# Kernel tuning notes

Measured on AMD Instinct MI355X. Metric: run time of the kernel, lower is better.

## Reference

```python
import jax, jax.numpy as jnp
import numpy as np

B, H, W = 2, 32, 128
HW = H * W
N, C = 4096, 64
KQ, KN = 32, 16          # nsample_q, nsample
DIST = 10.0              # neighbor distance threshold
NEG = -1e10


def _knn(q, p, k):
    # q: (B,M,3), p: (B,N,3) -> idx (B,M,k), sqdist (B,M,k)
    sqd = jnp.sum((q[:, :, None, :] - p[:, None, :, :]) ** 2, axis=-1)
    neg, idx = jax.lax.top_k(-sqd, k)
    return idx, -neg


def _gather(p, idx):
    # p: (B,N,C), idx: (B,M,K) -> (B,M,K,C)
    return jax.vmap(lambda a, i: a[i])(p, idx)


def _norm_feat(x):
    # per-point channel normalization, torch.std default is unbiased (ddof=1)
    m = jnp.mean(x, axis=-1, keepdims=True)
    s = jnp.clip(jnp.std(x, axis=-1, keepdims=True, ddof=1), 1e-12)
    return (x - m) / s


def _conv(x, w, b, g, e):
    # 1x1 conv + BatchNorm (track_running_stats=False -> batch stats) + LeakyReLU(0.1)
    y = jnp.einsum('bnkc,cd->bnkd', x, w) + b
    mu = y.mean(axis=(0, 1, 2), keepdims=True)
    var = y.var(axis=(0, 1, 2), keepdims=True)
    y = (y - mu) * jax.lax.rsqrt(var + 1e-5) * g + e
    return jnp.where(y > 0, y, 0.1 * y)


def setup_inputs() -> dict:
    key = jax.random.key(0)
    ks = jax.random.split(key, 20)
    inp = {
        'xyz_proj_raw': jax.random.normal(ks[0], (B, H, W, 3), jnp.float32),
        'warped_xyz': jax.random.normal(ks[1], (B, HW, 3), jnp.float32),
        'warped_points': jax.random.normal(ks[2], (B, HW, C), jnp.float32),
        'idx_n2': jax.random.randint(ks[3], (B, HW, 2), 0, W),
        'f2_xyz': jax.random.normal(ks[4], (B, N, 3), jnp.float32),
        'f2_points': jax.random.normal(ks[5], (B, N, C), jnp.float32),
        'lidar_z': jax.random.uniform(ks[6], (B, HW, 1), jnp.float32),
    }
    shapes = {
        'm1w0': (70, 128), 'm1w1': (128, 64), 'piw': (6, 64),
        'm2w0': (128, 64), 'm2w1': (64, 64), 'pcw': (10, 64),
        'm3w0': (192, 64), 'm3w1': (64, 64),
    }
    i = 7
    for name, shp in shapes.items():
        inp[name] = jax.random.normal(ks[i], shp, jnp.float32) * 0.05
        i += 1
        pre = name[:-2] if name[-2] == 'w' else name[:-1]
        suf = name[-1] if name[-2] == 'w' else ''
        cout = shp[1]
        inp[pre + 'b' + suf] = jnp.zeros((cout,), jnp.float32)
        inp[pre + 'g' + suf] = jnp.ones((cout,), jnp.float32)
        inp[pre + 'e' + suf] = jnp.zeros((cout,), jnp.float32)
    return inp


def reference(xyz_proj_raw, warped_xyz, warped_points, idx_n2, f2_xyz, f2_points, lidar_z,
              m1w0, m1b0, m1g0, m1e0, m1w1, m1b1, m1g1, m1e1,
              piw, pib, pig, pie,
              m2w0, m2b0, m2g0, m2e0, m2w1, m2b1, m2g1, m2e1,
              pcw, pcb, pcg, pce,
              m3w0, m3b0, m3g0, m3e0, m3w1, m3b1, m3g1, m3e1):
    # ---- stage 1: cross kNN grouping into image features ----
    idx_q, _ = _knn(warped_xyz, f2_xyz, KQ)
    qi_xyz = _gather(f2_xyz, idx_q)          # (B,HW,KQ,3)
    qi_pts = _gather(f2_points, idx_q)       # (B,HW,KQ,C)

    wxyz = warped_xyz * lidar_z              # (B,HW,3)
    pi_xyz_exp = jnp.broadcast_to(wxyz[:, :, None, :], (B, HW, KQ, 3))
    pi_pts_exp = jnp.broadcast_to(warped_points[:, :, None, :], (B, HW, KQ, C))
    pi_xyz_diff_concat = jnp.concatenate([pi_xyz_exp, qi_xyz], axis=3)  # (B,HW,KQ,6)

    pi_feat_diff = _norm_feat(pi_pts_exp) * _norm_feat(qi_pts)          # correlation
    feat = jnp.concatenate([pi_xyz_diff_concat, pi_feat_diff], axis=3)  # (B,HW,KQ,70)

    feat = _conv(feat, m1w0, m1b0, m1g0, m1e0)
    feat = _conv(feat, m1w1, m1b1, m1g1, m1e1)                          # (B,HW,KQ,64)
    pi_enc = _conv(pi_xyz_diff_concat, piw, pib, pig, pie)              # (B,HW,KQ,64)

    pi_cat = jnp.concatenate([pi_enc, feat], axis=3)
    pi_cat = _conv(pi_cat, m2w0, m2b0, m2g0, m2e0)
    pi_cat = _conv(pi_cat, m2w1, m2b1, m2g1, m2e1)
    WQ = jax.nn.softmax(pi_cat, axis=2)
    pi_feat1 = jnp.sum(WQ * feat, axis=2)                               # (B,HW,64)

    # ---- stage 2: self kNN (use_trans=False -> raw projected xyz), thresholded validity ----
    xyz_pr = xyz_proj_raw.reshape(B, HW, 3)
    idx2, sqd2 = _knn(xyz_pr, xyz_pr, KN)
    valid = (sqd2 < DIST * DIST).astype(pi_feat1.dtype)[..., None]      # (B,HW,KN,1)

    pc_xyz_g = _gather(wxyz, idx2)                                      # (B,HW,KN,3)
    pc_pts_g = _gather(pi_feat1, idx2)                                  # (B,HW,KN,64)
    pc_xyz_new = jnp.broadcast_to(wxyz[:, :, None, :], (B, HW, KN, 3))
    pc_pts_new = jnp.broadcast_to(warped_points[:, :, None, :], (B, HW, KN, C))

    pc_diff = pc_xyz_g - pc_xyz_new
    pc_euc = jnp.sqrt(jnp.sum(pc_diff * pc_diff, axis=3, keepdims=True) + 1e-20)
    pc_xyz_cat = jnp.concatenate([pc_xyz_new, pc_xyz_g, pc_diff, pc_euc], axis=3)  # 10ch

    pc_enc = _conv(pc_xyz_cat, pcw, pcb, pcg, pce)
    pc_cat = jnp.concatenate([pc_enc, pc_pts_new, pc_pts_g], axis=-1)   # (B,HW,KN,192)
    pc_cat = _conv(pc_cat, m3w0, m3b0, m3g0, m3e0)
    pc_cat = _conv(pc_cat, m3w1, m3b1, m3g1, m3e1)

    pc_cat = pc_cat * valid + NEG * (1.0 - valid)
    WP = jax.nn.softmax(pc_cat, axis=2)
    out = jnp.sum(WP * pc_pts_g, axis=2)                                # (B,HW,64)
    return out.reshape(B, H, W, -1)
```

## Files before the change

### kernel.cpp

```cpp
#include <hip/hip_runtime.h>
#include <math.h>

constexpr int Bn  = 2;
constexpr int HWn = 4096;
constexpr int Nn  = 4096;
constexpr int KQn = 32;
constexpr int KNn = 16;
constexpr float INV_R1 = 1.0f/262144.0f;
constexpr float INV_R2 = 1.0f/131072.0f;

typedef _Float16 f16x8 __attribute__((ext_vector_type(8)));
typedef float    f32x4 __attribute__((ext_vector_type(4)));

__device__ __forceinline__ float wred64(float v){
  #pragma unroll
  for (int m = 32; m > 0; m >>= 1) v += __shfl_xor(v, m, 64);
  return v;
}
__device__ __forceinline__ float leakyf(float v){ return v > 0.f ? v : 0.1f*v; }

__device__ __forceinline__ void bn_param(const float* st, int c, float inv_n,
                                         const float* g, const float* e,
                                         float& sc, float& sh){
  float mu  = st[c]*inv_n;
  float var = st[128+c]*inv_n - mu*mu;
  float s   = g[c]*rsqrtf(var + 1e-5f);
  sc = s; sh = e[c] - mu*s;
}

__device__ __forceinline__ void build_x70(int row,
    const float* __restrict__ wxyz, const float* __restrict__ f2_xyz,
    const float* __restrict__ normW, const float* __restrict__ normF2,
    const int* __restrict__ idxq, float* x){
  int p = row >> 5;
  int b = p >> 12;
  int idx = idxq[row];
  const float* wx = wxyz + (size_t)p*3;
  const float* fx = f2_xyz + ((size_t)b*Nn + idx)*3;
  x[0]=wx[0]; x[1]=wx[1]; x[2]=wx[2];
  x[3]=fx[0]; x[4]=fx[1]; x[5]=fx[2];
  const float4* nw = (const float4*)(normW  + (size_t)p*64);
  const float4* nf = (const float4*)(normF2 + ((size_t)b*Nn + idx)*64);
  #pragma unroll
  for (int c=0;c<16;c++){
    float4 a = nw[c], q = nf[c];
    x[6+4*c+0]=a.x*q.x; x[6+4*c+1]=a.y*q.y; x[6+4*c+2]=a.z*q.z; x[6+4*c+3]=a.w*q.w;
  }
}

__device__ __forceinline__ void build_x10(int row,
    const float* __restrict__ wxyz, const int* __restrict__ idx2, float* x){
  int p = row >> 4, b = p >> 12;
  int idx = idx2[row];
  const float* nw = wxyz + (size_t)p*3;
  const float* gw = wxyz + ((size_t)b*HWn + idx)*3;
  float n0=nw[0],n1=nw[1],n2=nw[2];
  float g0=gw[0],g1=gw[1],g2=gw[2];
  float d0=g0-n0, d1=g1-n1, d2=g2-n2;
  x[0]=n0;x[1]=n1;x[2]=n2; x[3]=g0;x[4]=g1;x[5]=g2;
  x[6]=d0;x[7]=d1;x[8]=d2; x[9]=sqrtf(d0*d0+d1*d1+d2*d2+1e-20f);
}

__global__ __launch_bounds__(256) void k_prep(
    const float* __restrict__ warped_xyz, const float* __restrict__ lidar_z,
    const float* __restrict__ warped_points, const float* __restrict__ f2_points,
    const float* __restrict__ m1w0, const float* __restrict__ m1w1,
    const float* __restrict__ piw, const float* __restrict__ pcw,
    const float* __restrict__ m2w0, const float* __restrict__ m2w1,
    const float* __restrict__ m3w0, const float* __restrict__ m3w1,
    float* __restrict__ wxyz, float* __restrict__ normW, float* __restrict__ normF2,
    float* __restrict__ piwT, float* __restrict__ pcwT,
    _Float16* __restrict__ w1h, _Float16* __restrict__ w2h,
    _Float16* __restrict__ w3h, _Float16* __restrict__ w4h,
    _Float16* __restrict__ w5h, _Float16* __restrict__ w6h)
{
  int blk = blockIdx.x, tid = threadIdx.x;
  if (blk < 4096){
    int lane = tid & 63;
    int p = blk*4 + (tid >> 6);
    const float* src; float* dst;
    if (p < Bn*HWn){ src = warped_points + (size_t)p*64; dst = normW + (size_t)p*64; }
    else { int q = p - Bn*HWn; src = f2_points + (size_t)q*64; dst = normF2 + (size_t)q*64; }
    float x = src[lane];
    float m = wred64(x) * (1.f/64.f);
    float d = x - m;
    float ss = wred64(d*d);
    float s = fmaxf(sqrtf(ss*(1.f/63.f)), 1e-12f);
    dst[lane] = d / s;
  } else if (blk < 4192){
    int e = (blk-4096)*256 + tid;
    wxyz[e] = warped_xyz[e] * lidar_z[e/3];
  } else if (blk < 4196){
    int e = (blk-4192)*256 + tid;
    if (e < 384){ piwT[(e & 63)*6  + (e >> 6)] = piw[e]; }
    else if (e < 1024){ int f = e-384; pcwT[(f & 63)*10 + (f >> 6)] = pcw[f]; }
  } else {
    int e = (blk-4196)*256 + tid;
    if (e < 12288){
      int j = e/96, k = e - j*96;
      w1h[e] = (k < 70) ? (_Float16)m1w0[k*128 + j] : (_Float16)0.f;
    } else if (e < 20480){
      int f = e - 12288; int d = f >> 7, c = f & 127;
      w2h[f] = (_Float16)m1w1[c*64 + d];
    } else if (e < 28672){
      int f = e - 20480; int d = f >> 7, c = f & 127;
      w3h[f] = (_Float16)m2w0[c*64 + d];
    } else if (e < 32768){
      int f = e - 28672; int d = f >> 6, c = f & 63;
      w4h[f] = (_Float16)m2w1[c*64 + d];
    } else if (e < 45056){
      int f = e - 32768; int d = f/192, c = f - 192*d;
      w5h[f] = (_Float16)m3w0[c*64 + d];
    } else {
      int f = e - 45056; int d = f >> 6, c = f & 63;
      w6h[f] = (_Float16)m3w1[c*64 + d];
    }
  }
}

template<int K, bool WRITE_VALID>
__global__ __launch_bounds__(256) void k_knn(
    const float* __restrict__ qpts, const float* __restrict__ pts,
    int* __restrict__ oidx, float* __restrict__ ovalid)
{
  __shared__ int hist[4*256];
  __shared__ int wsum[4];
  __shared__ unsigned int redm[4], redM[4];
  __shared__ unsigned int sh_sel;
  __shared__ int sh_rem, sh_cls, cnt_lt, cnt_eq;
  int b = blockIdx.x >> 12;
  int qi = blockIdx.x & 4095;
  int tid = threadIdx.x;
  int lane = tid & 63, wv = tid >> 6;
  const float* qp = qpts + ((size_t)(b*HWn+qi))*3;
  float qx=qp[0], qy=qp[1], qz=qp[2];
  const float* pb = pts + (size_t)b*Nn*3;
  unsigned int key[16];
  #pragma unroll
  for (int i=0;i<16;i++){
    int t = tid + i*256;
    float dx = __fsub_rn(qx, pb[t*3+0]);
    float dy = __fsub_rn(qy, pb[t*3+1]);
    float dz = __fsub_rn(qz, pb[t*3+2]);
    float d2 = __fadd_rn(__fadd_rn(__fmul_rn(dx,dx), __fmul_rn(dy,dy)), __fmul_rn(dz,dz));
    key[i] = __float_as_uint(d2);
  }
  unsigned int mn = key[0], mx = key[0];
  #pragma unroll
  for (int i=1;i<16;i++){ mn = min(mn, key[i]); mx = max(mx, key[i]); }
  #pragma unroll
  for (int m=32;m>0;m>>=1){
    mn = min(mn, (unsigned int)__shfl_xor((int)mn, m, 64));
    mx = max(mx, (unsigned int)__shfl_xor((int)mx, m, 64));
  }
  if (lane == 0){ redm[wv] = mn; redM[wv] = mx; }
  if (tid == 0){ cnt_lt = 0; cnt_eq = 0; }
  __syncthreads();
  mn = min(min(redm[0],redm[1]), min(redm[2],redm[3]));
  mx = max(max(redM[0],redM[1]), max(redM[2],redM[3]));
  unsigned int R = mx - mn;
  int L = (R == 0u) ? 0 : (31 - __clz(R));
  int shift = (L > 7) ? (L - 7) : 0;
  unsigned int dmask = 255u;

  unsigned int active = 0xFFFFu, below = 0u;
  int rem = K;
  for (;;){
    __syncthreads();
    #pragma unroll
    for (int j=0;j<4;j++) hist[j*256 + tid] = 0;
    __syncthreads();
    #pragma unroll
    for (int i=0;i<16;i++){
      if (active & (1u<<i))
        atomicAdd(&hist[wv*256 + (int)(((key[i]-mn) >> shift) & dmask)], 1);
    }
    __syncthreads();
    int h = hist[tid] + hist[256+tid] + hist[512+tid] + hist[768+tid];
    int pref = h;
    #pragma unroll
    for (int m=1;m<64;m<<=1){ int t = __shfl_up(pref, m, 64); if (lane >= m) pref += t; }
    if (lane == 63) wsum[wv] = pref;
    __syncthreads();
    int off = 0;
    #pragma unroll
    for (int i=0;i<3;i++) if (i < wv) off += wsum[i];
    pref += off;
    if (pref >= rem && (pref - h) < rem){
      sh_sel = (unsigned int)tid;
      sh_rem = rem - (pref - h);
      sh_cls = h;
    }
    __syncthreads();
    unsigned int sel = sh_sel; rem = sh_rem; int cls = sh_cls;
    #pragma unroll
    for (int i=0;i<16;i++){
      if (active & (1u<<i)){
        unsigned int d = ((key[i]-mn) >> shift) & dmask;
        if (d < sel) below |= (1u<<i);
        if (d != sel) active &= ~(1u<<i);
      }
    }
    if (cls == rem || shift == 0) break;
    int w = (shift < 8) ? shift : 8;
    shift -= w;
    dmask = (w == 8) ? 255u : ((1u<<w) - 1u);
  }
  size_t obase = ((size_t)(b*HWn+qi))*K;
  int nless = K - rem;
  const unsigned int U100 = __float_as_uint(100.0f);
  #pragma unroll
  for (int i=0;i<16;i++){
    if (below & (1u<<i)){
      int s = atomicAdd(&cnt_lt, 1);
      oidx[obase+s] = tid + i*256;
      if constexpr (WRITE_VALID) ovalid[obase+s] = (key[i] < U100) ? 1.f : 0.f;
    } else if (active & (1u<<i)){
      int s = atomicAdd(&cnt_eq, 1);
      if (s < rem){
        oidx[obase+nless+s] = tid + i*256;
        if constexpr (WRITE_VALID) ovalid[obase+nless+s] = (key[i] < U100) ? 1.f : 0.f;
      }
    }
  }
}

__global__ __launch_bounds__(256) void k_buildX1(
    const float* __restrict__ wxyz, const float* __restrict__ f2_xyz,
    const float* __restrict__ normW, const float* __restrict__ normF2,
    const int* __restrict__ idxq, _Float16* __restrict__ X1)
{
  int row = blockIdx.x*256 + threadIdx.x;
  float x[70];
  build_x70(row, wxyz, f2_xyz, normW, normF2, idxq, x);
  unsigned int* d32 = (unsigned int*)(X1 + (size_t)row*96);
  union { unsigned int u; _Float16 h[2]; } pk;
  #pragma unroll
  for (int c=0;c<35;c++){
    pk.h[0] = (_Float16)x[2*c]; pk.h[1] = (_Float16)x[2*c+1];
    d32[c] = pk.u;
  }
  #pragma unroll
  for (int c=35;c<48;c++) d32[c] = 0u;
}

__global__ __launch_bounds__(256) void k_gram(
    const float* __restrict__ wxyz, const float* __restrict__ f2_xyz,
    const int* __restrict__ idxq, const int* __restrict__ idx2,
    float* __restrict__ gram)
{
  __shared__ float sacc[66];
  int blk = blockIdx.x, tid = threadIdx.x, lane = tid & 63;
  if (blk < 64){
    float a[28];
    #pragma unroll
    for (int q=0;q<28;q++) a[q]=0.f;
    int g = blk*256 + tid;
    for (int s=0;s<16;s++){
      int row = g + s*16384;
      int p = row >> 5, b = p >> 12;
      int idx = idxq[row];
      const float* wx = wxyz + (size_t)p*3;
      const float* fx = f2_xyz + ((size_t)b*Nn + idx)*3;
      float xt[7] = {wx[0],wx[1],wx[2],fx[0],fx[1],fx[2],1.f};
      int q=0;
      #pragma unroll
      for (int i=0;i<7;i++)
        #pragma unroll
        for (int j=i;j<7;j++) a[q++] += xt[i]*xt[j];
    }
    if (tid < 28) sacc[tid]=0.f;
    __syncthreads();
    #pragma unroll
    for (int q=0;q<28;q++){
      float v = wred64(a[q]);
      if (lane==0) atomicAdd(&sacc[q], v);
    }
    __syncthreads();
    if (tid < 28) atomicAdd(&gram[tid], sacc[tid]);
  } else {
    float a[66];
    #pragma unroll
    for (int q=0;q<66;q++) a[q]=0.f;
    int g = (blk-64)*256 + tid;
    for (int s=0;s<16;s++){
      int row = g + s*8192;
      float x[10];
      build_x10(row, wxyz, idx2, x);
      float xt[11] = {x[0],x[1],x[2],x[3],x[4],x[5],x[6],x[7],x[8],x[9],1.f};
      int q=0;
      #pragma unroll
      for (int i=0;i<11;i++)
        #pragma unroll
        for (int j=i;j<11;j++) a[q++] += xt[i]*xt[j];
    }
    if (tid < 66) sacc[tid]=0.f;
    __syncthreads();
    #pragma unroll
    for (int q=0;q<66;q++){
      float v = wred64(a[q]);
      if (lane==0) atomicAdd(&sacc[q], v);
    }
    __syncthreads();
    if (tid < 66) atomicAdd(&gram[32+tid], sacc[tid]);
  }
}

__global__ __launch_bounds__(128) void k_gram_fin(
    const float* __restrict__ gram,
    const float* __restrict__ piw, const float* __restrict__ pib,
    const float* __restrict__ pcw, const float* __restrict__ pcb,
    float* stats)
{
  int tid = threadIdx.x;
  if (tid < 64){
    int c = tid;
    float wt[7];
    #pragma unroll
    for (int i=0;i<6;i++) wt[i] = piw[i*64+c];
    wt[6] = pib[c];
    const float* G = gram;
    float sum=0.f, ssq=0.f;
    #pragma unroll
    for (int i=0;i<7;i++){
      int offi = i*7 - (i*(i-1))/2;
      sum += wt[i]*G[offi + (6-i)];
      #pragma unroll
      for (int j=0;j<7;j++){
        int ii = i<j? i : j, jj = i<j? j : i;
        int o = ii*7 - (ii*(ii-1))/2 + (jj-ii);
        ssq += wt[i]*wt[j]*G[o];
      }
    }
    stats[2*256+c] = sum; stats[2*256+128+c] = ssq;
  } else {
    int c = tid-64;
    float wt[11];
    #pragma unroll
    for (int i=0;i<10;i++) wt[i] = pcw[i*64+c];
    wt[10] = pcb[c];
    const float* G = gram + 32;
    float sum=0.f, ssq=0.f;
    #pragma unroll
    for (int i=0;i<11;i++){
      int offi = i*11 - (i*(i-1))/2;
      sum += wt[i]*G[offi + (10-i)];
      #pragma unroll
      for (int j=0;j<11;j++){
        int ii = i<j? i : j, jj = i<j? j : i;
        int o = ii*11 - (ii*(ii-1))/2 + (jj-ii);
        ssq += wt[i]*wt[j]*G[o];
      }
    }
    stats[5*256+c] = sum; stats[5*256+128+c] = ssq;
  }
}

__global__ __launch_bounds__(256) void k_mfma_stats1(
    const _Float16* __restrict__ X1, const _Float16* __restrict__ w1h,
    float* stats)
{
  __shared__ float ssum[128], sssq[128];
  int tid = threadIdx.x;
  if (tid < 128){ ssum[tid]=0.f; sssq[tid]=0.f; }
  __syncthreads();
  int wave = tid >> 6, lane = tid & 63;
  int quad = lane >> 4, n16 = lane & 15;
  float r1[8], r2[8];
  #pragma unroll
  for (int i=0;i<8;i++){ r1[i]=0.f; r2[i]=0.f; }
  for (int t=0;t<4;t++){
    int m0 = blockIdx.x*256 + t*64 + wave*16;
    const _Float16* xr = X1 + (size_t)(m0 + n16)*96 + quad*8;
    f16x8 a0 = *(const f16x8*)(xr);
    f16x8 a1 = *(const f16x8*)(xr + 32);
    f16x8 a2 = *(const f16x8*)(xr + 64);
    #pragma unroll
    for (int nt = 0; nt < 8; nt++){
      const _Float16* wr = w1h + (size_t)(nt*16 + n16)*96 + quad*8;
      f16x8 b0 = *(const f16x8*)(wr);
      f16x8 b1 = *(const f16x8*)(wr + 32);
      f16x8 b2 = *(const f16x8*)(wr + 64);
      f32x4 acc = {0.f,0.f,0.f,0.f};
      acc = __builtin_amdgcn_mfma_f32_16x16x32_f16(a0, b0, acc, 0,0,0);
      acc = __builtin_amdgcn_mfma_f32_16x16x32_f16(a1, b1, acc, 0,0,0);
      acc = __builtin_amdgcn_mfma_f32_16x16x32_f16(a2, b2, acc, 0,0,0);
      float s1 = acc[0]+acc[1]+acc[2]+acc[3];
      float s2 = acc[0]*acc[0]+acc[1]*acc[1]+acc[2]*acc[2]+acc[3]*acc[3];
      s1 += __shfl_xor(s1, 16, 64); s1 += __shfl_xor(s1, 32, 64);
      s2 += __shfl_xor(s2, 16, 64); s2 += __shfl_xor(s2, 32, 64);
      r1[nt] += s1; r2[nt] += s2;
    }
  }
  if (quad == 0){
    #pragma unroll
    for (int nt=0;nt<8;nt++){
      atomicAdd(&ssum[nt*16+n16], r1[nt]); atomicAdd(&sssq[nt*16+n16], r2[nt]);
    }
  }
  __syncthreads();
  if (tid < 128){ atomicAdd(&stats[tid], ssum[tid]); atomicAdd(&stats[128+tid], sssq[tid]); }
}

__global__ __launch_bounds__(256) void k_mfma_m1(
    const _Float16* __restrict__ X1, const _Float16* __restrict__ w1h,
    const _Float16* __restrict__ w2h,
    const float* __restrict__ m1g0, const float* __restrict__ m1e0,
    float* stats, _Float16* __restrict__ y2h)
{
  __shared__ _Float16 st[64*136];
  __shared__ float sc1[128], sh1[128], ssum[64], sssq[64];
  int tid = threadIdx.x;
  if (tid < 128){
    float s,h; bn_param(stats, tid, INV_R1, m1g0, m1e0, s, h);
    sc1[tid]=s; sh1[tid]=h;
  }
  if (tid < 64){ ssum[tid]=0.f; sssq[tid]=0.f; }
  __syncthreads();
  int wave = tid >> 6, lane = tid & 63;
  int quad = lane >> 4, n16 = lane & 15;
  float r1[4], r2[4];
  #pragma unroll
  for (int i=0;i<4;i++){ r1[i]=0.f; r2[i]=0.f; }
  for (int t=0;t<4;t++){
    int m0 = blockIdx.x*256 + t*64 + wave*16;
    const _Float16* xr = X1 + (size_t)(m0 + n16)*96 + quad*8;
    f16x8 a0 = *(const f16x8*)(xr);
    f16x8 a1 = *(const f16x8*)(xr + 32);
    f16x8 a2 = *(const f16x8*)(xr + 64);
    #pragma unroll
    for (int nt = 0; nt < 8; nt++){
      const _Float16* wr = w1h + (size_t)(nt*16 + n16)*96 + quad*8;
      f16x8 b0 = *(const f16x8*)(wr);
      f16x8 b1 = *(const f16x8*)(wr + 32);
      f16x8 b2 = *(const f16x8*)(wr + 64);
      f32x4 acc = {0.f,0.f,0.f,0.f};
      acc = __builtin_amdgcn_mfma_f32_16x16x32_f16(a0, b0, acc, 0,0,0);
      acc = __builtin_amdgcn_mfma_f32_16x16x32_f16(a1, b1, acc, 0,0,0);
      acc = __builtin_amdgcn_mfma_f32_16x16x32_f16(a2, b2, acc, 0,0,0);
      int ch = nt*16 + n16;
      float sc = sc1[ch], sh = sh1[ch];
      #pragma unroll
      for (int r=0;r<4;r++){
        float v = leakyf(acc[r]*sc + sh);
        st[(size_t)(wave*16 + quad*4 + r)*136 + ch] = (_Float16)v;
      }
    }
    __syncthreads();
    const _Float16* tr = st + (size_t)(wave*16 + n16)*136 + quad*8;
    f16x8 t0 = *(const f16x8*)(tr);
    f16x8 t1 = *(const f16x8*)(tr + 32);
    f16x8 t2 = *(const f16x8*)(tr + 64);
    f16x8 t3 = *(const f16x8*)(tr + 96);
    #pragma unroll
    for (int nt = 0; nt < 4; nt++){
      const _Float16* wr = w2h + (size_t)(nt*16 + n16)*128 + quad*8;
      f16x8 b0 = *(const f16x8*)(wr);
      f16x8 b1 = *(const f16x8*)(wr + 32);
      f16x8 b2 = *(const f16x8*)(wr + 64);
      f16x8 b3 = *(const f16x8*)(wr + 96);
      f32x4 acc = {0.f,0.f,0.f,0.f};
      acc = __builtin_amdgcn_mfma_f32_16x16x32_f16(t0, b0, acc, 0,0,0);
      acc = __builtin_amdgcn_mfma_f32_16x16x32_f16(t1, b1, acc, 0,0,0);
      acc = __builtin_amdgcn_mfma_f32_16x16x32_f16(t2, b2, acc, 0,0,0);
      acc = __builtin_amdgcn_mfma_f32_16x16x32_f16(t3, b3, acc, 0,0,0);
      int ch = nt*16 + n16;
      #pragma unroll
      for (int r=0;r<4;r++){
        int rowg = blockIdx.x*256 + t*64 + wave*16 + quad*4 + r;
        y2h[(size_t)rowg*64 + ch] = (_Float16)acc[r];
      }
      float s1 = acc[0]+acc[1]+acc[2]+acc[3];
      float s2 = acc[0]*acc[0]+acc[1]*acc[1]+acc[2]*acc[2]+acc[3]*acc[3];
      s1 += __shfl_xor(s1, 16, 64); s1 += __shfl_xor(s1, 32, 64);
      s2 += __shfl_xor(s2, 16, 64); s2 += __shfl_xor(s2, 32, 64);
      r1[nt] += s1; r2[nt] += s2;
    }
    __syncthreads();
  }
  if (quad == 0){
    #pragma unroll
    for (int nt=0;nt<4;nt++){
      atomicAdd(&ssum[nt*16+n16], r1[nt]); atomicAdd(&sssq[nt*16+n16], r2[nt]);
    }
  }
  __syncthreads();
  if (tid < 64){ atomicAdd(&stats[1*256+tid], ssum[tid]); atomicAdd(&stats[1*256+128+tid], sssq[tid]); }
}

__global__ __launch_bounds__(256) void k_mfma_m2a(
    const float* __restrict__ wxyz, const float* __restrict__ f2_xyz,
    const int* __restrict__ idxq,
    const float* __restrict__ piwT, const float* __restrict__ pib,
    const float* __restrict__ pig, const float* __restrict__ pie,
    const float* __restrict__ m1g1, const float* __restrict__ m1e1,
    const _Float16* __restrict__ y2h, const _Float16* __restrict__ w3h,
    float* stats, _Float16* __restrict__ y3h)
{
  __shared__ _Float16 su[64*136];
  __shared__ float spw[384];
  __shared__ float scp[64], shp[64], sc2[64], sh2[64], ssum[64], sssq[64];
  int tid = threadIdx.x;
  for (int d = tid; d < 384; d += 256) spw[d] = piwT[d];
  if (tid < 64){
    float s,h;
    bn_param(stats+2*256, tid, INV_R1, pig,  pie,  s, h); scp[tid]=s; shp[tid]=h;
    bn_param(stats+1*256, tid, INV_R1, m1g1, m1e1, s, h); sc2[tid]=s; sh2[tid]=h;
    ssum[tid]=0.f; sssq[tid]=0.f;
  }
  __syncthreads();
  int r = tid & 63, cg = tid >> 6;
  int wave = tid >> 6, lane = tid & 63, quad = lane >> 4, n16 = lane & 15;
  float r1[4], r2[4];
  #pragma unroll
  for (int i=0;i<4;i++){ r1[i]=0.f; r2[i]=0.f; }
  for (int t=0;t<4;t++){
    int rowg = blockIdx.x*256 + t*64 + r;
    {
      int p = rowg >> 5, b = p >> 12;
      int idx = idxq[rowg];
      const float* wx = wxyz + (size_t)p*3;
      const float* fx = f2_xyz + ((size_t)b*Nn + idx)*3;
      float x0=wx[0],x1=wx[1],x2=wx[2],x3=fx[0],x4=fx[1],x5=fx[2];
      #pragma unroll
      for (int jj=0;jj<16;jj++){
        int j = cg*16 + jj;
        const float* pw = spw + j*6;
        float e = pib[j] + x0*pw[0]+x1*pw[1]+x2*pw[2]+x3*pw[3]+x4*pw[4]+x5*pw[5];
        su[r*136 + j] = (_Float16)leakyf(e*scp[j] + shp[j]);
      }
      const f16x8* yr = (const f16x8*)(y2h + (size_t)rowg*64 + cg*16);
      f16x8 q0 = yr[0], q1 = yr[1];
      #pragma unroll
      for (int jj=0;jj<8;jj++){
        int c = cg*16 + jj;
        su[r*136 + 64 + c] = (_Float16)leakyf((float)q0[jj]*sc2[c] + sh2[c]);
      }
      #pragma unroll
      for (int jj=0;jj<8;jj++){
        int c = cg*16 + 8 + jj;
        su[r*136 + 64 + c] = (_Float16)leakyf((float)q1[jj]*sc2[c] + sh2[c]);
      }
    }
    __syncthreads();
    const _Float16* ur = su + (size_t)(wave*16 + n16)*136 + quad*8;
    f16x8 a0 = *(const f16x8*)(ur);
    f16x8 a1 = *(const f16x8*)(ur + 32);
    f16x8 a2 = *(const f16x8*)(ur + 64);
    f16x8 a3 = *(const f16x8*)(ur + 96);
    #pragma unroll
    for (int nt = 0; nt < 4; nt++){
      const _Float16* wr = w3h + (size_t)(nt*16 + n16)*128 + quad*8;
      f16x8 b0 = *(const f16x8*)(wr);
      f16x8 b1 = *(const f16x8*)(wr + 32);
      f16x8 b2 = *(const f16x8*)(wr + 64);
      f16x8 b3 = *(const f16x8*)(wr + 96);
      f32x4 acc = {0.f,0.f,0.f,0.f};
      acc = __builtin_amdgcn_mfma_f32_16x16x32_f16(a0, b0, acc, 0,0,0);
      acc = __builtin_amdgcn_mfma_f32_16x16x32_f16(a1, b1, acc, 0,0,0);
      acc = __builtin_amdgcn_mfma_f32_16x16x32_f16(a2, b2, acc, 0,0,0);
      acc = __builtin_amdgcn_mfma_f32_16x16x32_f16(a3, b3, acc, 0,0,0);
      int ch = nt*16 + n16;
      #pragma unroll
      for (int rr=0;rr<4;rr++){
        int rg = blockIdx.x*256 + t*64 + wave*16 + quad*4 + rr;
        y3h[(size_t)rg*64 + ch] = (_Float16)acc[rr];
      }
      float s1 = acc[0]+acc[1]+acc[2]+acc[3];
      float s2 = acc[0]*acc[0]+acc[1]*acc[1]+acc[2]*acc[2]+acc[3]*acc[3];
      s1 += __shfl_xor(s1, 16, 64); s1 += __shfl_xor(s1, 32, 64);
      s2 += __shfl_xor(s2, 16, 64); s2 += __shfl_xor(s2, 32, 64);
      r1[nt] += s1; r2[nt] += s2;
    }
    __syncthreads();
  }
  if (quad == 0){
    #pragma unroll
    for (int nt=0;nt<4;nt++){
      atomicAdd(&ssum[nt*16+n16], r1[nt]); atomicAdd(&sssq[nt*16+n16], r2[nt]);
    }
  }
  __syncthreads();
  if (tid < 64){ atomicAdd(&stats[3*256+tid], ssum[tid]); atomicAdd(&stats[3*256+128+tid], sssq[tid]); }
}

__global__ __launch_bounds__(256) void k_mfma_pw64(
    const _Float16* __restrict__ yin, const _Float16* __restrict__ wh,
    const float* __restrict__ g, const float* __restrict__ e,
    const float* statsIn, float* statsOut, float inv_n,
    _Float16* __restrict__ yout)
{
  __shared__ _Float16 stt[64*72];
  __shared__ float sc[64], sh[64], ssum[64], sssq[64];
  int tid = threadIdx.x;
  if (tid < 64){
    float s,h; bn_param(statsIn, tid, inv_n, g, e, s, h);
    sc[tid]=s; sh[tid]=h; ssum[tid]=0.f; sssq[tid]=0.f;
  }
  __syncthreads();
  int r = tid & 63, cg = tid >> 6;
  int wave = tid >> 6, lane = tid & 63, quad = lane >> 4, n16 = lane & 15;
  float r1[4], r2[4];
  #pragma unroll
  for (int i=0;i<4;i++){ r1[i]=0.f; r2[i]=0.f; }
  for (int t=0;t<4;t++){
    int rowg = blockIdx.x*256 + t*64 + r;
    const f16x8* yr = (const f16x8*)(yin + (size_t)rowg*64 + cg*16);
    f16x8 q0 = yr[0], q1 = yr[1];
    #pragma unroll
    for (int jj=0;jj<8;jj++){
      int c = cg*16 + jj;
      stt[r*72 + c] = (_Float16)leakyf((float)q0[jj]*sc[c] + sh[c]);
    }
    #pragma unroll
    for (int jj=0;jj<8;jj++){
      int c = cg*16 + 8 + jj;
      stt[r*72 + c] = (_Float16)leakyf((float)q1[jj]*sc[c] + sh[c]);
    }
    __syncthreads();
    const _Float16* tr = stt + (size_t)(wave*16 + n16)*72 + quad*8;
    f16x8 a0 = *(const f16x8*)(tr);
    f16x8 a1 = *(const f16x8*)(tr + 32);
    #pragma unroll
    for (int nt = 0; nt < 4; nt++){
      const _Float16* wr = wh + (size_t)(nt*16 + n16)*64 + quad*8;
      f16x8 b0 = *(const f16x8*)(wr);
      f16x8 b1 = *(const f16x8*)(wr + 32);
      f32x4 acc = {0.f,0.f,0.f,0.f};
      acc = __builtin_amdgcn_mfma_f32_16x16x32_f16(a0, b0, acc, 0,0,0);
      acc = __builtin_amdgcn_mfma_f32_16x16x32_f16(a1, b1, acc, 0,0,0);
      int ch = nt*16 + n16;
      #pragma unroll
      for (int rr=0;rr<4;rr++){
        int rg = blockIdx.x*256 + t*64 + wave*16 + quad*4 + rr;
        yout[(size_t)rg*64 + ch] = (_Float16)acc[rr];
      }
      float s1 = acc[0]+acc[1]+acc[2]+acc[3];
      float s2 = acc[0]*acc[0]+acc[1]*acc[1]+acc[2]*acc[2]+acc[3]*acc[3];
      s1 += __shfl_xor(s1, 16, 64); s1 += __shfl_xor(s1, 32, 64);
      s2 += __shfl_xor(s2, 16, 64); s2 += __shfl_xor(s2, 32, 64);
      r1[nt] += s1; r2[nt] += s2;
    }
    __syncthreads();
  }
  if (quad == 0){
    #pragma unroll
    for (int nt=0;nt<4;nt++){
      atomicAdd(&ssum[nt*16+n16], r1[nt]); atomicAdd(&sssq[nt*16+n16], r2[nt]);
    }
  }
  __syncthreads();
  if (tid < 64){ atomicAdd(&statsOut[tid], ssum[tid]); atomicAdd(&statsOut[128+tid], sssq[tid]); }
}

__global__ __launch_bounds__(256) void k_mfma_m3a(
    const float* __restrict__ wxyz, const float* __restrict__ warped_points,
    const _Float16* __restrict__ pif1h, const int* __restrict__ idx2,
    const float* __restrict__ pcwT, const float* __restrict__ pcb,
    const float* __restrict__ pcg, const float* __restrict__ pce,
    const _Float16* __restrict__ w5h,
    float* stats, _Float16* __restrict__ y5h)
{
  __shared__ _Float16 sv[64*200];
  __shared__ float spw[640];
  __shared__ float scp[64], shp[64], ssum[64], sssq[64];
  int tid = threadIdx.x;
  for (int d = tid; d < 640; d += 256) spw[d] = pcwT[d];
  if (tid < 64){
    float s,h; bn_param(stats+5*256, tid, INV_R2, pcg, pce, s, h);
    scp[tid]=s; shp[tid]=h; ssum[tid]=0.f; sssq[tid]=0.f;
  }
  __syncthreads();
  int r = tid & 63, cg = tid >> 6;
  int wave = tid >> 6, lane = tid & 63, quad = lane >> 4, n16 = lane & 15;
  float r1[4], r2[4];
  #pragma unroll
  for (int i=0;i<4;i++){ r1[i]=0.f; r2[i]=0.f; }
  for (int t=0;t<4;t++){
    int rowg = blockIdx.x*256 + t*64 + r;
    {
      int p = rowg >> 4, b = p >> 12;
      int idx = idx2[rowg];
      float x[10];
      build_x10(rowg, wxyz, idx2, x);
      #pragma unroll
      for (int jj=0;jj<16;jj++){
        int j = cg*16 + jj;
        const float* pw = spw + j*10;
        float e = pcb[j];
        #pragma unroll
        for (int i=0;i<10;i++) e += x[i]*pw[i];
        sv[r*200 + j] = (_Float16)leakyf(e*scp[j] + shp[j]);
      }
      const float4* wp = (const float4*)(warped_points + (size_t)p*64 + cg*16);
      #pragma unroll
      for (int v4=0; v4<4; v4++){
        float4 q = wp[v4];
        int c = 64 + cg*16 + v4*4;
        sv[r*200 + c + 0] = (_Float16)q.x;
        sv[r*200 + c + 1] = (_Float16)q.y;
        sv[r*200 + c + 2] = (_Float16)q.z;
        sv[r*200 + c + 3] = (_Float16)q.w;
      }
      const f16x8* pg = (const f16x8*)(pif1h + ((size_t)(b*HWn) + idx)*64 + cg*16);
      f16x8 g0 = pg[0], g1 = pg[1];
      #pragma unroll
      for (int jj=0;jj<8;jj++) sv[r*200 + 128 + cg*16 + jj] = g0[jj];
      #pragma unroll
      for (int jj=0;jj<8;jj++) sv[r*200 + 136 + cg*16 + jj] = g1[jj];
    }
    __syncthreads();
    const _Float16* vr = sv + (size_t)(wave*16 + n16)*200 + quad*8;
    f16x8 a0 = *(const f16x8*)(vr);
    f16x8 a1 = *(const f16x8*)(vr + 32);
    f16x8 a2 = *(const f16x8*)(vr + 64);
    f16x8 a3 = *(const f16x8*)(vr + 96);
    f16x8 a4 = *(const f16x8*)(vr + 128);
    f16x8 a5 = *(const f16x8*)(vr + 160);
    #pragma unroll
    for (int nt = 0; nt < 4; nt++){
      const _Float16* wr = w5h + (size_t)(nt*16 + n16)*192 + quad*8;
      f32x4 acc = {0.f,0.f,0.f,0.f};
      acc = __builtin_amdgcn_mfma_f32_16x16x32_f16(a0, *(const f16x8*)(wr),       acc, 0,0,0);
      acc = __builtin_amdgcn_mfma_f32_16x16x32_f16(a1, *(const f16x8*)(wr + 32),  acc, 0,0,0);
      acc = __builtin_amdgcn_mfma_f32_16x16x32_f16(a2, *(const f16x8*)(wr + 64),  acc, 0,0,0);
      acc = __builtin_amdgcn_mfma_f32_16x16x32_f16(a3, *(const f16x8*)(wr + 96),  acc, 0,0,0);
      acc = __builtin_amdgcn_mfma_f32_16x16x32_f16(a4, *(const f16x8*)(wr + 128), acc, 0,0,0);
      acc = __builtin_amdgcn_mfma_f32_16x16x32_f16(a5, *(const f16x8*)(wr + 160), acc, 0,0,0);
      int ch = nt*16 + n16;
      #pragma unroll
      for (int rr=0;rr<4;rr++){
        int rg = blockIdx.x*256 + t*64 + wave*16 + quad*4 + rr;
        y5h[(size_t)rg*64 + ch] = (_Float16)acc[rr];
      }
      float s1 = acc[0]+acc[1]+acc[2]+acc[3];
      float s2 = acc[0]*acc[0]+acc[1]*acc[1]+acc[2]*acc[2]+acc[3]*acc[3];
      s1 += __shfl_xor(s1, 16, 64); s1 += __shfl_xor(s1, 32, 64);
      s2 += __shfl_xor(s2, 16, 64); s2 += __shfl_xor(s2, 32, 64);
      r1[nt] += s1; r2[nt] += s2;
    }
    __syncthreads();
  }
  if (quad == 0){
    #pragma unroll
    for (int nt=0;nt<4;nt++){
      atomicAdd(&ssum[nt*16+n16], r1[nt]); atomicAdd(&sssq[nt*16+n16], r2[nt]);
    }
  }
  __syncthreads();
  if (tid < 64){ atomicAdd(&stats[6*256+tid], ssum[tid]); atomicAdd(&stats[6*256+128+tid], sssq[tid]); }
}

__global__ __launch_bounds__(256) void k_softmax1(
    const _Float16* __restrict__ y2h, const _Float16* __restrict__ y4h,
    const float* stats,
    const float* __restrict__ m1g1, const float* __restrict__ m1e1,
    const float* __restrict__ m2g1, const float* __restrict__ m2e1,
    _Float16* __restrict__ pif1h)
{
  int tid = threadIdx.x, lane = tid & 63;
  int p = blockIdx.x*4 + (tid >> 6);
  int d = lane;
  float sc2,sh2,sc4,sh4;
  bn_param(stats+1*256, d, INV_R1, m1g1, m1e1, sc2, sh2);
  bn_param(stats+4*256, d, INV_R1, m2g1, m2e1, sc4, sh4);
  size_t rb = (size_t)p*KQn;
  float v[32]; float mx = -1e30f;
  #pragma unroll
  for (int k=0;k<32;k++){
    float t = leakyf((float)y4h[(rb+k)*64 + d]*sc4 + sh4);
    v[k] = t; mx = fmaxf(mx, t);
  }
  float se = 0.f;
  #pragma unroll
  for (int k=0;k<32;k++){ float ev = __expf(v[k]-mx); v[k]=ev; se += ev; }
  float inv = 1.f/se, acc = 0.f;
  #pragma unroll
  for (int k=0;k<32;k++){
    float f = leakyf((float)y2h[(rb+k)*64 + d]*sc2 + sh2);
    acc += v[k]*f;
  }
  pif1h[(size_t)p*64 + d] = (_Float16)(acc*inv);
}

__global__ __launch_bounds__(256) void k_softmax2(
    const _Float16* __restrict__ y6h, const _Float16* __restrict__ pif1h,
    const int* __restrict__ idx2, const float* __restrict__ validf,
    const float* stats,
    const float* __restrict__ m3g1, const float* __restrict__ m3e1,
    float* __restrict__ out)
{
  int tid = threadIdx.x, lane = tid & 63;
  int p = blockIdx.x*4 + (tid >> 6);
  int b = p >> 12;
  int d = lane;
  float sc,sh; bn_param(stats+7*256, d, INV_R2, m3g1, m3e1, sc, sh);
  size_t rb = (size_t)p*KNn;
  float v[16]; float mx = -1e30f;
  #pragma unroll
  for (int k=0;k<16;k++){
    float t = leakyf((float)y6h[(rb+k)*64 + d]*sc + sh);
    t = (validf[rb+k] > 0.5f) ? t : -1e10f;
    v[k] = t; mx = fmaxf(mx, t);
  }
  float se = 0.f;
  #pragma unroll
  for (int k=0;k<16;k++){ float ev = __expf(v[k]-mx); v[k]=ev; se += ev; }
  float inv = 1.f/se, acc = 0.f;
  #pragma unroll
  for (int k=0;k<16;k++){
    int idx = idx2[rb+k];
    acc += v[k]*(float)pif1h[((size_t)(b*HWn) + idx)*64 + d];
  }
  out[(size_t)p*64 + d] = acc*inv;
}

extern "C" void kernel_launch(void* const* d_in, const int* in_sizes, int n_in,
                              void* d_out, int out_size, void* d_ws, size_t ws_size,
                              hipStream_t stream)
{
  (void)in_sizes; (void)n_in; (void)out_size; (void)ws_size;
  const float* xyz_proj      = (const float*)d_in[0];
  const float* warped_xyz    = (const float*)d_in[1];
  const float* warped_points = (const float*)d_in[2];
  const float* f2_xyz        = (const float*)d_in[4];
  const float* f2_points     = (const float*)d_in[5];
  const float* lidar_z       = (const float*)d_in[6];
  const float* m1w0=(const float*)d_in[7],  *m1g0=(const float*)d_in[9],  *m1e0=(const float*)d_in[10];
  const float* m1w1=(const float*)d_in[11], *m1g1=(const float*)d_in[13], *m1e1=(const float*)d_in[14];
  const float* piw =(const float*)d_in[15], *pib =(const float*)d_in[16], *pig =(const float*)d_in[17], *pie =(const float*)d_in[18];
  const float* m2w0=(const float*)d_in[19], *m2g0=(const float*)d_in[21], *m2e0=(const float*)d_in[22];
  const float* m2w1=(const float*)d_in[23], *m2g1=(const float*)d_in[25], *m2e1=(const float*)d_in[26];
  const float* pcw =(const float*)d_in[27], *pcb =(const float*)d_in[28], *pcg =(const float*)d_in[29], *pce =(const float*)d_in[30];
  const float* m3w0=(const float*)d_in[31], *m3g0=(const float*)d_in[33], *m3e0=(const float*)d_in[34];
  const float* m3w1=(const float*)d_in[35], *m3g1=(const float*)d_in[37], *m3e1=(const float*)d_in[38];
  float* out = (float*)d_out;

  float* ws     = (float*)d_ws;
  float* wxyz   = ws;
  float* normW  = wxyz   + 24576;
  float* normF2 = normW  + 524288;
  float* piwT   = normF2 + 524288;
  float* pcwT   = piwT   + 384;
  float* stats  = pcwT   + 640;
  float* gram   = stats  + 2048;
  int*   idxq   = (int*)(gram + 128);
  int*   idx2   = idxq   + 262144;
  float* validf = (float*)(idx2 + 131072);
  _Float16* pif1h = (_Float16*)(validf + 131072);
  float* X1f    = validf + 131072 + 524288;
  _Float16* X1  = (_Float16*)X1f;
  float* y2f    = X1f + 12582912;
  _Float16* y2h = (_Float16*)y2f;
  float* y3f    = y2f + 8388608;
  _Float16* y3h = (_Float16*)y3f;
  float* whb    = y3f + 8388608;
  _Float16* w1h = (_Float16*)whb;
  _Float16* w2h = w1h + 12288;
  _Float16* w3h = w2h + 8192;
  _Float16* w4h = w3h + 8192;
  _Float16* w5h = w4h + 4096;
  _Float16* w6h = w5h + 12288;
  _Float16* y4h = (_Float16*)X1f;
  _Float16* y5h = (_Float16*)(X1f + 8388608);
  _Float16* y6h = y3h;

  hipMemsetAsync(stats, 0, (2048+128)*sizeof(float), stream);
  k_prep<<<4388,256,0,stream>>>(warped_xyz, lidar_z, warped_points, f2_points,
                                m1w0, m1w1, piw, pcw, m2w0, m2w1, m3w0, m3w1,
                                wxyz, normW, normF2, piwT, pcwT,
                                w1h, w2h, w3h, w4h, w5h, w6h);
  k_knn<32,false><<<8192,256,0,stream>>>(warped_xyz, f2_xyz, idxq, nullptr);
  k_knn<16,true ><<<8192,256,0,stream>>>(xyz_proj, xyz_proj, idx2, validf);
  k_buildX1<<<1024,256,0,stream>>>(wxyz, f2_xyz, normW, normF2, idxq, X1);
  k_gram<<<96,256,0,stream>>>(wxyz, f2_xyz, idxq, idx2, gram);
  k_gram_fin<<<1,128,0,stream>>>(gram, piw, pib, pcw, pcb, stats);
  k_mfma_stats1<<<1024,256,0,stream>>>(X1, w1h, stats);
  k_mfma_m1<<<1024,256,0,stream>>>(X1, w1h, w2h, m1g0, m1e0, stats, y2h);
  k_mfma_m2a<<<1024,256,0,stream>>>(wxyz, f2_xyz, idxq, piwT, pib, pig, pie,
                                    m1g1, m1e1, y2h, w3h, stats, y3h);
  k_mfma_pw64<<<1024,256,0,stream>>>(y3h, w4h, m2g0, m2e0,
                                     stats+3*256, stats+4*256, INV_R1, y4h);
  k_softmax1<<<2048,256,0,stream>>>(y2h, y4h, stats, m1g1, m1e1, m2g1, m2e1, pif1h);
  k_mfma_m3a<<<512,256,0,stream>>>(wxyz, warped_points, pif1h, idx2,
                                   pcwT, pcb, pcg, pce, w5h, stats, y5h);
  k_mfma_pw64<<<512,256,0,stream>>>(y5h, w6h, m3g0, m3e0,
                                    stats+6*256, stats+7*256, INV_R2, y6h);
  k_softmax2<<<2048,256,0,stream>>>(y6h, pif1h, idx2, validf, stats, m3g1, m3e1, out);
}
```

Before: 576.4 us.

## Vectorize kNN point loads and fuse X1 build, gram and stats1 kernels

The kNN kernel now has each thread load 16 contiguous points as twelve float4 loads instead of strided scalar loads, and the emitted index mapping changes to tid*16+i to match. The X1 build, gram accumulation and first-layer MFMA statistics kernels are merged into a single launch. Each block reads back the X1 rows it just wrote, which relies on global writes being visible across waves after __syncthreads. This removes two launches and some X1 re-reads from cold cache. The change in tie ordering among equal distances could alter which neighbors are selected when keys tie.

```diff
diff --git a/kernel.cpp b/kernel.cpp
--- a/kernel.cpp
+++ b/kernel.cpp
@@ -136,14 +136,20 @@
   float qx=qp[0], qy=qp[1], qz=qp[2];
   const float* pb = pts + (size_t)b*Nn*3;
   unsigned int key[16];
-  #pragma unroll
-  for (int i=0;i<16;i++){
-    int t = tid + i*256;
-    float dx = __fsub_rn(qx, pb[t*3+0]);
-    float dy = __fsub_rn(qy, pb[t*3+1]);
-    float dz = __fsub_rn(qz, pb[t*3+2]);
-    float d2 = __fadd_rn(__fadd_rn(__fmul_rn(dx,dx), __fmul_rn(dy,dy)), __fmul_rn(dz,dz));
-    key[i] = __float_as_uint(d2);
+  {
+    const float4* pb4 = (const float4*)(pb + (size_t)tid*48);
+    float4 v[12];
+    #pragma unroll
+    for (int i=0;i<12;i++) v[i] = pb4[i];
+    const float* f = (const float*)v;
+    #pragma unroll
+    for (int i=0;i<16;i++){
+      float dx = __fsub_rn(qx, f[i*3+0]);
+      float dy = __fsub_rn(qy, f[i*3+1]);
+      float dz = __fsub_rn(qz, f[i*3+2]);
+      float d2 = __fadd_rn(__fadd_rn(__fmul_rn(dx,dx), __fmul_rn(dy,dy)), __fmul_rn(dz,dz));
+      key[i] = __float_as_uint(d2);
+    }
   }
   unsigned int mn = key[0], mx = key[0];
   #pragma unroll
@@ -213,49 +219,86 @@
   for (int i=0;i<16;i++){
     if (below & (1u<<i)){
       int s = atomicAdd(&cnt_lt, 1);
-      oidx[obase+s] = tid + i*256;
+      oidx[obase+s] = tid*16 + i;
       if constexpr (WRITE_VALID) ovalid[obase+s] = (key[i] < U100) ? 1.f : 0.f;
     } else if (active & (1u<<i)){
       int s = atomicAdd(&cnt_eq, 1);
       if (s < rem){
-        oidx[obase+nless+s] = tid + i*256;
+        oidx[obase+nless+s] = tid*16 + i;
         if constexpr (WRITE_VALID) ovalid[obase+nless+s] = (key[i] < U100) ? 1.f : 0.f;
       }
     }
   }
 }
 
-__global__ __launch_bounds__(256) void k_buildX1(
+__global__ __launch_bounds__(256) void k_build_stats(
     const float* __restrict__ wxyz, const float* __restrict__ f2_xyz,
     const float* __restrict__ normW, const float* __restrict__ normF2,
-    const int* __restrict__ idxq, _Float16* __restrict__ X1)
-{
-  int row = blockIdx.x*256 + threadIdx.x;
-  float x[70];
-  build_x70(row, wxyz, f2_xyz, normW, normF2, idxq, x);
-  unsigned int* d32 = (unsigned int*)(X1 + (size_t)row*96);
-  union { unsigned int u; _Float16 h[2]; } pk;
-  #pragma unroll
-  for (int c=0;c<35;c++){
-    pk.h[0] = (_Float16)x[2*c]; pk.h[1] = (_Float16)x[2*c+1];
-    d32[c] = pk.u;
-  }
-  #pragma unroll
-  for (int c=35;c<48;c++) d32[c] = 0u;
-}
-
-__global__ __launch_bounds__(256) void k_gram(
-    const float* __restrict__ wxyz, const float* __restrict__ f2_xyz,
     const int* __restrict__ idxq, const int* __restrict__ idx2,
-    float* __restrict__ gram)
-{
+    const _Float16* __restrict__ w1h,
+    _Float16* __restrict__ X1, float* stats, float* __restrict__ gram)
+{
+  __shared__ float ssum[128], sssq[128];
   __shared__ float sacc[66];
   int blk = blockIdx.x, tid = threadIdx.x, lane = tid & 63;
-  if (blk < 64){
+  if (blk < 1024){
+    int row = blk*256 + tid;
+    {
+      float x[70];
+      build_x70(row, wxyz, f2_xyz, normW, normF2, idxq, x);
+      unsigned int* d32 = (unsigned int*)(X1 + (size_t)row*96);
+      union { unsigned int u; _Float16 h[2]; } pk;
+      #pragma unroll
+      for (int c=0;c<35;c++){
+        pk.h[0] = (_Float16)x[2*c]; pk.h[1] = (_Float16)x[2*c+1];
+        d32[c] = pk.u;
+      }
+      #pragma unroll
+      for (int c=35;c<48;c++) d32[c] = 0u;
+    }
+    if (tid < 128){ ssum[tid]=0.f; sssq[tid]=0.f; }
+    __syncthreads();
+    int wave = tid >> 6;
+    int quad = lane >> 4, n16 = lane & 15;
+    float r1[8], r2[8];
+    #pragma unroll
+    for (int i=0;i<8;i++){ r1[i]=0.f; r2[i]=0.f; }
+    for (int t=0;t<4;t++){
+      int m0 = blk*256 + t*64 + wave*16;
+      const _Float16* xr = X1 + (size_t)(m0 + n16)*96 + quad*8;
+      f16x8 a0 = *(const f16x8*)(xr);
+      f16x8 a1 = *(const f16x8*)(xr + 32);
+      f16x8 a2 = *(const f16x8*)(xr + 64);
+      #pragma unroll
+      for (int nt = 0; nt < 8; nt++){
+        const _Float16* wr = w1h + (size_t)(nt*16 + n16)*96 + quad*8;
+        f16x8 b0 = *(const f16x8*)(wr);
+        f16x8 b1 = *(const f16x8*)(wr + 32);
+        f16x8 b2 = *(const f16x8*)(wr + 64);
+        f32x4 acc = {0.f,0.f,0.f,0.f};
+        acc = __builtin_amdgcn_mfma_f32_16x16x32_f16(a0, b0, acc, 0,0,0);
+        acc = __builtin_amdgcn_mfma_f32_16x16x32_f16(a1, b1, acc, 0,0,0);
+        acc = __builtin_amdgcn_mfma_f32_16x16x32_f16(a2, b2, acc, 0,0,0);
+        float s1 = acc[0]+acc[1]+acc[2]+acc[3];
+        float s2 = acc[0]*acc[0]+acc[1]*acc[1]+acc[2]*acc[2]+acc[3]*acc[3];
+        s1 += __shfl_xor(s1, 16, 64); s1 += __shfl_xor(s1, 32, 64);
+        s2 += __shfl_xor(s2, 16, 64); s2 += __shfl_xor(s2, 32, 64);
+        r1[nt] += s1; r2[nt] += s2;
+      }
+    }
+    if (quad == 0){
+      #pragma unroll
+      for (int nt=0;nt<8;nt++){
+        atomicAdd(&ssum[nt*16+n16], r1[nt]); atomicAdd(&sssq[nt*16+n16], r2[nt]);
+      }
+    }
+    __syncthreads();
+    if (tid < 128){ atomicAdd(&stats[tid], ssum[tid]); atomicAdd(&stats[128+tid], sssq[tid]); }
+  } else if (blk < 1088){
     float a[28];
     #pragma unroll
     for (int q=0;q<28;q++) a[q]=0.f;
-    int g = blk*256 + tid;
+    int g = (blk-1024)*256 + tid;
     for (int s=0;s<16;s++){
       int row = g + s*16384;
       int p = row >> 5, b = p >> 12;
@@ -282,7 +325,7 @@
     float a[66];
     #pragma unroll
     for (int q=0;q<66;q++) a[q]=0.f;
-    int g = (blk-64)*256 + tid;
+    int g = (blk-1088)*256 + tid;
     for (int s=0;s<16;s++){
       int row = g + s*8192;
       float x[10];
@@ -354,52 +397,6 @@
     }
     stats[5*256+c] = sum; stats[5*256+128+c] = ssq;
   }
-}
-
-__global__ __launch_bounds__(256) void k_mfma_stats1(
-    const _Float16* __restrict__ X1, const _Float16* __restrict__ w1h,
-    float* stats)
-{
-  __shared__ float ssum[128], sssq[128];
-  int tid = threadIdx.x;
-  if (tid < 128){ ssum[tid]=0.f; sssq[tid]=0.f; }
-  __syncthreads();
-  int wave = tid >> 6, lane = tid & 63;
-  int quad = lane >> 4, n16 = lane & 15;
-  float r1[8], r2[8];
-  #pragma unroll
-  for (int i=0;i<8;i++){ r1[i]=0.f; r2[i]=0.f; }
-  for (int t=0;t<4;t++){
-    int m0 = blockIdx.x*256 + t*64 + wave*16;
-    const _Float16* xr = X1 + (size_t)(m0 + n16)*96 + quad*8;
-    f16x8 a0 = *(const f16x8*)(xr);
-    f16x8 a1 = *(const f16x8*)(xr + 32);
-    f16x8 a2 = *(const f16x8*)(xr + 64);
-    #pragma unroll
-    for (int nt = 0; nt < 8; nt++){
-      const _Float16* wr = w1h + (size_t)(nt*16 + n16)*96 + quad*8;
-      f16x8 b0 = *(const f16x8*)(wr);
-      f16x8 b1 = *(const f16x8*)(wr + 32);
-      f16x8 b2 = *(const f16x8*)(wr + 64);
-      f32x4 acc = {0.f,0.f,0.f,0.f};
-      acc = __builtin_amdgcn_mfma_f32_16x16x32_f16(a0, b0, acc, 0,0,0);
-      acc = __builtin_amdgcn_mfma_f32_16x16x32_f16(a1, b1, acc, 0,0,0);
-      acc = __builtin_amdgcn_mfma_f32_16x16x32_f16(a2, b2, acc, 0,0,0);
-      float s1 = acc[0]+acc[1]+acc[2]+acc[3];
-      float s2 = acc[0]*acc[0]+acc[1]*acc[1]+acc[2]*acc[2]+acc[3]*acc[3];
-      s1 += __shfl_xor(s1, 16, 64); s1 += __shfl_xor(s1, 32, 64);
-      s2 += __shfl_xor(s2, 16, 64); s2 += __shfl_xor(s2, 32, 64);
-      r1[nt] += s1; r2[nt] += s2;
-    }
-  }
-  if (quad == 0){
-    #pragma unroll
-    for (int nt=0;nt<8;nt++){
-      atomicAdd(&ssum[nt*16+n16], r1[nt]); atomicAdd(&sssq[nt*16+n16], r2[nt]);
-    }
-  }
-  __syncthreads();
-  if (tid < 128){ atomicAdd(&stats[tid], ssum[tid]); atomicAdd(&stats[128+tid], sssq[tid]); }
 }
 
 __global__ __launch_bounds__(256) void k_mfma_m1(
@@ -872,10 +869,9 @@
                                 w1h, w2h, w3h, w4h, w5h, w6h);
   k_knn<32,false><<<8192,256,0,stream>>>(warped_xyz, f2_xyz, idxq, nullptr);
   k_knn<16,true ><<<8192,256,0,stream>>>(xyz_proj, xyz_proj, idx2, validf);
-  k_buildX1<<<1024,256,0,stream>>>(wxyz, f2_xyz, normW, normF2, idxq, X1);
-  k_gram<<<96,256,0,stream>>>(wxyz, f2_xyz, idxq, idx2, gram);
+  k_build_stats<<<1120,256,0,stream>>>(wxyz, f2_xyz, normW, normF2, idxq, idx2,
+                                       w1h, X1, stats, gram);
   k_gram_fin<<<1,128,0,stream>>>(gram, piw, pib, pcw, pcb, stats);
-  k_mfma_stats1<<<1024,256,0,stream>>>(X1, w1h, stats);
   k_mfma_m1<<<1024,256,0,stream>>>(X1, w1h, w2h, m1g0, m1e0, stats, y2h);
   k_mfma_m2a<<<1024,256,0,stream>>>(wxyz, f2_xyz, idxq, piwT, pib, pig, pie,
                                     m1g1, m1e1, y2h, w3h, stats, y3h);
```

Measured after the change: 548.3 us. -4.9%, faster.
